# Performance work log

Measured on AMD Instinct MI355X. Metric: run time of the kernel, lower is better.

Reference implementation:

```python
import jax, jax.numpy as jnp
import numpy as np

N = 100000   # total atoms in the batch
E = 400000   # directed edges (bonds both directions)
F = 11       # raw atom feature dim (Linear(11, vector_dim))
D = 512      # vector_dim
L = 5        # num_conv_layers
G = 2048     # number of molecules (graphs) in the batch


def setup_inputs() -> dict:
    key = jax.random.key(0)
    k = jax.random.split(key, 6)
    x = jax.random.uniform(k[0], (N, F), dtype=jnp.float32)  # nonneg counts-like features
    edge_index = jax.random.randint(k[1], (2, E), 0, N, dtype=jnp.int32)
    batch = jnp.sort(jax.random.randint(k[2], (N,), 0, G, dtype=jnp.int32))
    exp_W = jax.random.normal(k[3], (F, D), dtype=jnp.float32) * (1.0 / np.sqrt(F))
    exp_b = jnp.zeros((D,), dtype=jnp.float32)
    gcn_W = jax.random.normal(k[4], (L, D, D), dtype=jnp.float32) * (1.0 / np.sqrt(D))
    gcn_b = jnp.zeros((L, D), dtype=jnp.float32)
    return {"x": x, "edge_index": edge_index, "batch": batch,
            "exp_W": exp_W, "exp_b": exp_b, "gcn_W": gcn_W, "gcn_b": gcn_b}


def reference(x, edge_index, batch, exp_W, exp_b, gcn_W, gcn_b):
    # GraphEmbedding.forward (eval mode: dropout = identity)
    src, dst = edge_index[0], edge_index[1]
    h = jnp.log(x + 1.0) @ exp_W + exp_b  # expansion Linear(11, D)  -> [N, D]

    # GCN normalization with improved=True: self-loop weight 2.0
    # deg_i = sum of incoming edge weights (1.0) + 2.0 self-loop
    ones_e = jnp.ones((E,), dtype=h.dtype)
    deg = jax.ops.segment_sum(ones_e, dst, num_segments=N) + 2.0
    dinv = jax.lax.rsqrt(deg)              # deg >= 2, always finite
    enorm = dinv[src] * dinv[dst]          # per-edge norm (weight 1.0)
    self_norm = 2.0 * dinv * dinv          # self-loop norm (weight 2.0)

    for l in range(L):
        xw = h @ gcn_W[l]                                   # [N, D]
        msg = enorm[:, None] * xw[src]                      # gather + scale, [E, D]
        agg = jax.ops.segment_sum(msg, dst, num_segments=N)  # scatter-add
        agg = agg + self_norm[:, None] * xw + gcn_b[l]
        h = h + jax.nn.relu(agg)                            # residual + relu (dropout off)

    # global_add_pool over molecules
    return jax.ops.segment_sum(h, batch, num_segments=G)    # [G, D]
```

## Files before the change

kernel.cpp:

```cpp
#include <hip/hip_runtime.h>
#include <hip/hip_bf16.h>
#include <stdint.h>

typedef __attribute__((ext_vector_type(8))) short bf16x8;
typedef __attribute__((ext_vector_type(4))) float f32x4;
typedef unsigned short ushort_t;
typedef unsigned int uint_t;

__device__ __forceinline__ unsigned short f2bf(float f) {
  unsigned u = __float_as_uint(f);
  u += 0x7fffu + ((u >> 16) & 1u);
  return (unsigned short)(u >> 16);
}
__device__ __forceinline__ float bf2f(unsigned u16) {
  return __uint_as_float(u16 << 16);
}
__device__ __forceinline__ void fma8(float* a, uint4 u, float w) {
  a[0] += w * bf2f(u.x & 0xffffu); a[1] += w * bf2f(u.x >> 16);
  a[2] += w * bf2f(u.y & 0xffffu); a[3] += w * bf2f(u.y >> 16);
  a[4] += w * bf2f(u.z & 0xffffu); a[5] += w * bf2f(u.z >> 16);
  a[6] += w * bf2f(u.w & 0xffffu); a[7] += w * bf2f(u.w >> 16);
}
__device__ __forceinline__ uint4 pack8u(const float* a) {
  uint4 p;
  p.x = (uint_t)f2bf(a[0]) | ((uint_t)f2bf(a[1]) << 16);
  p.y = (uint_t)f2bf(a[2]) | ((uint_t)f2bf(a[3]) << 16);
  p.z = (uint_t)f2bf(a[4]) | ((uint_t)f2bf(a[5]) << 16);
  p.w = (uint_t)f2bf(a[6]) | ((uint_t)f2bf(a[7]) << 16);
  return p;
}

__global__ void k_zero(int* __restrict__ p, int n) {
  int i = blockIdx.x * blockDim.x + threadIdx.x;
  if (i < n) p[i] = 0;
}

__global__ void k_prep_w(const float* __restrict__ W, ushort_t* __restrict__ Wt, int total) {
  int idx = blockIdx.x * blockDim.x + threadIdx.x;
  if (idx >= total) return;
  int j   = idx & 7;
  int col = (idx >> 3) & 127;
  int kg  = (idx >> 10) & 3;
  int kt  = (idx >> 12) & 15;
  int nt  = (idx >> 16) & 3;
  int l   = idx >> 18;
  int k = kt * 32 + kg * 8 + j;
  int n = nt * 128 + col;
  Wt[idx] = f2bf(W[((size_t)(l * 512 + k)) * 512 + n]);
}

__global__ __launch_bounds__(256) void k_expand(const float* __restrict__ x,
                                                const float* __restrict__ eW,
                                                const float* __restrict__ eb,
                                                ushort_t* __restrict__ h, int N) {
  const int wid = (blockIdx.x * 256 + threadIdx.x) >> 6;
  const int nw = (gridDim.x * 256) >> 6;
  const int l = threadIdx.x & 63;

  float wf[11][8];
  float bias[8];
#pragma unroll
  for (int f = 0; f < 11; ++f) {
    float4 a = *(const float4*)&eW[f * 512 + l * 8];
    float4 b = *(const float4*)&eW[f * 512 + l * 8 + 4];
    wf[f][0] = a.x; wf[f][1] = a.y; wf[f][2] = a.z; wf[f][3] = a.w;
    wf[f][4] = b.x; wf[f][5] = b.y; wf[f][6] = b.z; wf[f][7] = b.w;
  }
  {
    float4 a = *(const float4*)&eb[l * 8];
    float4 b = *(const float4*)&eb[l * 8 + 4];
    bias[0] = a.x; bias[1] = a.y; bias[2] = a.z; bias[3] = a.w;
    bias[4] = b.x; bias[5] = b.y; bias[6] = b.z; bias[7] = b.w;
  }

  for (int n = wid; n < N; n += nw) {
    float xv = (l < 11) ? x[(size_t)n * 11 + l] : 0.f;
    float lx = log1pf(xv);
    float acc[8];
#pragma unroll
    for (int j = 0; j < 8; ++j) acc[j] = bias[j];
#pragma unroll
    for (int f = 0; f < 11; ++f) {
      float c = __shfl(lx, f, 64);
#pragma unroll
      for (int j = 0; j < 8; ++j) acc[j] += c * wf[f][j];
    }
    *(uint4*)(h + (size_t)n * 512 + l * 8) = pack8u(acc);
  }
}

__global__ void k_deg(const int* __restrict__ dst, int* __restrict__ deg, int E) {
  int e = blockIdx.x * blockDim.x + threadIdx.x;
  if (e < E) atomicAdd(&deg[dst[e]], 1);
}

__global__ void k_dinv(const int* __restrict__ deg, float* __restrict__ dinv,
                       float* __restrict__ selfn, int N) {
  int n = blockIdx.x * blockDim.x + threadIdx.x;
  if (n >= N) return;
  float d = (float)deg[n] + 2.0f;
  dinv[n] = rsqrtf(d);
  selfn[n] = 2.0f / d;
}

__global__ void k_scan_a(const int* __restrict__ deg, int* __restrict__ off,
                         int* __restrict__ bsum, int N) {
  __shared__ int sd[256];
  int t = threadIdx.x;
  int i0 = blockIdx.x * 1024 + t * 4;
  int d[4];
#pragma unroll
  for (int j = 0; j < 4; ++j) d[j] = (i0 + j < N) ? deg[i0 + j] : 0;
  int ts = d[0] + d[1] + d[2] + d[3];
  sd[t] = ts;
  __syncthreads();
  for (int o = 1; o < 256; o <<= 1) {
    int v = (t >= o) ? sd[t - o] : 0;
    __syncthreads();
    sd[t] += v;
    __syncthreads();
  }
  int incl = sd[t];
  int run = incl - ts;
#pragma unroll
  for (int j = 0; j < 4; ++j) {
    if (i0 + j < N) off[i0 + j] = run;
    run += d[j];
  }
  if (t == 255) bsum[blockIdx.x] = incl;
}

__global__ void k_scan_b(const int* __restrict__ bsum, int* __restrict__ bpre, int nb,
                         int* __restrict__ off, int N, int E) {
  __shared__ int sd[256];
  int t = threadIdx.x;
  int v = (t < nb) ? bsum[t] : 0;
  sd[t] = v;
  __syncthreads();
  for (int o = 1; o < 256; o <<= 1) {
    int u = (t >= o) ? sd[t - o] : 0;
    __syncthreads();
    sd[t] += u;
    __syncthreads();
  }
  if (t < nb) bpre[t] = sd[t] - v;
  if (t == 0) off[N] = E;
}

__global__ void k_scan_c(int* __restrict__ off, const int* __restrict__ bpre, int N) {
  int i = blockIdx.x * blockDim.x + threadIdx.x;
  if (i < N) off[i] += bpre[i >> 10];
}

__global__ void k_fill(const int* __restrict__ src, const int* __restrict__ dst,
                       const int* __restrict__ off, int* __restrict__ cur,
                       int* __restrict__ ssrc, int E) {
  int e = blockIdx.x * blockDim.x + threadIdx.x;
  if (e >= E) return;
  int t = dst[e];
  int p = atomicAdd(&cur[t], 1);
  ssrc[off[t] + p] = src[e];
}

__global__ __launch_bounds__(256) void k_agg2(const ushort_t* __restrict__ h,
                                              ushort_t* __restrict__ s,
                                              const int* __restrict__ off,
                                              const int* __restrict__ ssrc,
                                              const float* __restrict__ dinv,
                                              const float* __restrict__ selfn, int N) {
  const int wid = (blockIdx.x * 256 + threadIdx.x) >> 6;
  const int nw = (gridDim.x * 256) >> 6;
  const int l = threadIdx.x & 63;

  for (int n0 = wid * 2; n0 < N; n0 += nw * 2) {
    const int n1 = n0 + 1;
    const bool v1 = n1 < N;
    int i0 = off[n0], e0 = off[n0 + 1];
    int i1 = v1 ? e0 : 0, e1 = v1 ? off[n1 + 1] : 0;
    float dn0 = dinv[n0], dn1 = v1 ? dinv[n1] : 0.f;
    float a0[8], a1[8];
    {
      uint4 u = *(const uint4*)(h + (size_t)n0 * 512 + l * 8);
      float sn = selfn[n0];
      a0[0] = sn * bf2f(u.x & 0xffffu); a0[1] = sn * bf2f(u.x >> 16);
      a0[2] = sn * bf2f(u.y & 0xffffu); a0[3] = sn * bf2f(u.y >> 16);
      a0[4] = sn * bf2f(u.z & 0xffffu); a0[5] = sn * bf2f(u.z >> 16);
      a0[6] = sn * bf2f(u.w & 0xffffu); a0[7] = sn * bf2f(u.w >> 16);
    }
#pragma unroll
    for (int j = 0; j < 8; ++j) a1[j] = 0.f;
    if (v1) {
      uint4 u = *(const uint4*)(h + (size_t)n1 * 512 + l * 8);
      fma8(a1, u, selfn[n1]);
    }
    while (i0 < e0 && i1 < e1) {
      int m0 = ssrc[i0++], m1 = ssrc[i1++];
      float w0 = dn0 * dinv[m0], w1 = dn1 * dinv[m1];
      uint4 u0 = *(const uint4*)(h + (size_t)m0 * 512 + l * 8);
      uint4 u1 = *(const uint4*)(h + (size_t)m1 * 512 + l * 8);
      fma8(a0, u0, w0);
      fma8(a1, u1, w1);
    }
    while (i0 < e0) {
      int m0 = ssrc[i0++];
      float w0 = dn0 * dinv[m0];
      uint4 u0 = *(const uint4*)(h + (size_t)m0 * 512 + l * 8);
      fma8(a0, u0, w0);
    }
    while (i1 < e1) {
      int m1 = ssrc[i1++];
      float w1 = dn1 * dinv[m1];
      uint4 u1 = *(const uint4*)(h + (size_t)m1 * 512 + l * 8);
      fma8(a1, u1, w1);
    }
    *(uint4*)(s + (size_t)n0 * 512 + l * 8) = pack8u(a0);
    if (v1) *(uint4*)(s + (size_t)n1 * 512 + l * 8) = pack8u(a1);
  }
}

__global__ __launch_bounds__(256) void k_gemm(const ushort_t* __restrict__ s,
                                              const ushort_t* __restrict__ Wt,
                                              const float* __restrict__ gbl,
                                              ushort_t* __restrict__ h, int N) {
  __shared__ alignas(16) ushort_t smem[8192];
  ushort_t* Alds = smem;
  ushort_t* Blds = smem + 4096;
  const int tid = threadIdx.x;
  const int m0 = blockIdx.x * 128;
  const int nt = blockIdx.y;
  const int wv = tid >> 6, ln = tid & 63;
  const int wrow = wv >> 1, wcol = wv & 1;
  const int l15 = ln & 15, l4 = ln >> 4;

  f32x4 acc[4][4];
#pragma unroll
  for (int i = 0; i < 4; ++i)
#pragma unroll
    for (int j = 0; j < 4; ++j) acc[i][j] = (f32x4){0.f, 0.f, 0.f, 0.f};

  const int arow0 = tid >> 2, apiece = tid & 3;
  const int grow0 = min(m0 + arow0, N - 1);
  const int grow1 = min(m0 + 64 + arow0, N - 1);

  for (int kt = 0; kt < 16; ++kt) {
    __syncthreads();
    {
      const ushort_t* p0 = s + (size_t)grow0 * 512 + kt * 32 + apiece * 8;
      const ushort_t* p1 = s + (size_t)grow1 * 512 + kt * 32 + apiece * 8;
      __builtin_amdgcn_global_load_lds(
          (const __attribute__((address_space(1))) uint_t*)p0,
          (__attribute__((address_space(3))) uint_t*)&Alds[tid * 8], 16, 0, 0);
      __builtin_amdgcn_global_load_lds(
          (const __attribute__((address_space(1))) uint_t*)p1,
          (__attribute__((address_space(3))) uint_t*)&Alds[(256 + tid) * 8], 16, 0, 0);
    }
    {
      const ushort_t* wt = Wt + (((size_t)nt * 16 + kt) << 12);
      const ushort_t* g1 = wt + (tid << 3);
      __builtin_amdgcn_global_load_lds(
          (const __attribute__((address_space(1))) uint_t*)g1,
          (__attribute__((address_space(3))) uint_t*)&Blds[tid * 8], 16, 0, 0);
      __builtin_amdgcn_global_load_lds(
          (const __attribute__((address_space(1))) uint_t*)(g1 + 2048),
          (__attribute__((address_space(3))) uint_t*)&Blds[(256 + tid) * 8], 16, 0, 0);
    }
    __syncthreads();
    bf16x8 a[4], b[4];
#pragma unroll
    for (int i = 0; i < 4; ++i)
      a[i] = *(const bf16x8*)&Alds[(wrow * 64 + i * 16 + l15) * 32 + l4 * 8];
#pragma unroll
    for (int j = 0; j < 4; ++j)
      b[j] = *(const bf16x8*)&Blds[(l4 * 128 + wcol * 64 + j * 16 + l15) * 8];
#pragma unroll
    for (int i = 0; i < 4; ++i)
#pragma unroll
      for (int j = 0; j < 4; ++j)
        acc[i][j] = __builtin_amdgcn_mfma_f32_16x16x32_bf16(a[i], b[j], acc[i][j], 0, 0, 0);
  }

  float* cst = (float*)smem;
  __syncthreads();
#pragma unroll
  for (int p = 0; p < 4; ++p) {
    const int wrow_sel = p >> 1, ipair = (p & 1) * 2;
    if (wrow == wrow_sel) {
#pragma unroll
      for (int ii = 0; ii < 2; ++ii) {
        int i = ipair + ii;
#pragma unroll
        for (int v = 0; v < 4; ++v) {
          int r32 = ii * 16 + l4 * 4 + v;
#pragma unroll
          for (int j = 0; j < 4; ++j)
            cst[r32 * 128 + wcol * 64 + j * 16 + l15] = acc[i][j][v];
        }
      }
    }
    __syncthreads();
#pragma unroll
    for (int k = 0; k < 2; ++k) {
      int u = k * 256 + tid;
      int row_l = u >> 4, cb = u & 15;
      int grow = m0 + wrow_sel * 64 + ipair * 16 + row_l;
      if (grow < N) {
        float4 c0 = *(const float4*)&cst[row_l * 128 + cb * 8];
        float4 c1 = *(const float4*)&cst[row_l * 128 + cb * 8 + 4];
        float c[8] = {c0.x, c0.y, c0.z, c0.w, c1.x, c1.y, c1.z, c1.w};
        const float* gp = gbl + nt * 128 + cb * 8;
        float4 b0 = *(const float4*)gp;
        float4 b1 = *(const float4*)(gp + 4);
        float bb[8] = {b0.x, b0.y, b0.z, b0.w, b1.x, b1.y, b1.z, b1.w};
        ushort_t* hp = h + (size_t)grow * 512 + nt * 128 + cb * 8;
        uint4 hu = *(const uint4*)hp;
        float hv[8];
        hv[0] = bf2f(hu.x & 0xffffu); hv[1] = bf2f(hu.x >> 16);
        hv[2] = bf2f(hu.y & 0xffffu); hv[3] = bf2f(hu.y >> 16);
        hv[4] = bf2f(hu.z & 0xffffu); hv[5] = bf2f(hu.z >> 16);
        hv[6] = bf2f(hu.w & 0xffffu); hv[7] = bf2f(hu.w >> 16);
#pragma unroll
        for (int j = 0; j < 8; ++j) hv[j] += fmaxf(c[j] + bb[j], 0.f);
        *(uint4*)hp = pack8u(hv);
      }
    }
    __syncthreads();
  }
}

__device__ __forceinline__ int lbound(const int* a, int n, int v) {
  int lo = 0, hi = n;
  while (lo < hi) {
    int m = (lo + hi) >> 1;
    if (a[m] < v) lo = m + 1; else hi = m;
  }
  return lo;
}

__global__ __launch_bounds__(256) void k_pool(const ushort_t* __restrict__ h,
                                              const int* __restrict__ batch,
                                              float* __restrict__ out, int N) {
  __shared__ float red[4 * 512];
  int g = blockIdx.x;
  int t = threadIdx.x;
  int w = t >> 6, l = t & 63;
  int start = lbound(batch, N, g);
  int end = lbound(batch, N, g + 1);
  float acc[8];
#pragma unroll
  for (int j = 0; j < 8; ++j) acc[j] = 0.f;
  for (int n = start + w; n < end; n += 4) {
    uint4 u = *(const uint4*)(h + (size_t)n * 512 + l * 8);
    acc[0] += bf2f(u.x & 0xffffu); acc[1] += bf2f(u.x >> 16);
    acc[2] += bf2f(u.y & 0xffffu); acc[3] += bf2f(u.y >> 16);
    acc[4] += bf2f(u.z & 0xffffu); acc[5] += bf2f(u.z >> 16);
    acc[6] += bf2f(u.w & 0xffffu); acc[7] += bf2f(u.w >> 16);
  }
#pragma unroll
  for (int j = 0; j < 8; ++j) red[w * 512 + l * 8 + j] = acc[j];
  __syncthreads();
  if (t < 128) {
    float4 sv = make_float4(0.f, 0.f, 0.f, 0.f);
#pragma unroll
    for (int ww = 0; ww < 4; ++ww) {
      float4 v = *(const float4*)&red[ww * 512 + t * 4];
      sv.x += v.x; sv.y += v.y; sv.z += v.z; sv.w += v.w;
    }
    *(float4*)&out[(size_t)g * 512 + t * 4] = sv;
  }
}

extern "C" void kernel_launch(void* const* d_in, const int* in_sizes, int n_in,
                              void* d_out, int out_size, void* d_ws, size_t ws_size,
                              hipStream_t stream) {
  const float* x  = (const float*)d_in[0];
  const int* ei   = (const int*)d_in[1];
  const int* batch= (const int*)d_in[2];
  const float* eW = (const float*)d_in[3];
  const float* eb = (const float*)d_in[4];
  const float* gW = (const float*)d_in[5];
  const float* gb = (const float*)d_in[6];
  float* out = (float*)d_out;

  const int N = in_sizes[0] / 11;
  const int E = in_sizes[1] / 2;
  const int G = out_size / 512;
  const int L = in_sizes[5] / (512 * 512);

  const int* src = ei;
  const int* dst = ei + E;

  char* p = (char*)d_ws;
  auto carve = [&](size_t bytes) {
    char* q = p;
    p += (bytes + 255) & ~(size_t)255;
    return q;
  };
  ushort_t* h         = (ushort_t*)carve((size_t)N * 512 * 2);
  ushort_t* s         = (ushort_t*)carve((size_t)N * 512 * 2);
  ushort_t* Wt        = (ushort_t*)carve((size_t)L * 512 * 512 * 2);
  int* deg            = (int*)carve((size_t)N * 4);
  float* dinv         = (float*)carve((size_t)N * 4);
  float* selfn        = (float*)carve((size_t)N * 4);
  int* off            = (int*)carve(((size_t)N + 1) * 4);
  int* cur            = (int*)carve((size_t)N * 4);
  int* ssrc           = (int*)carve((size_t)E * 4);
  int* bsum           = (int*)carve(1024);
  int* bpre           = (int*)carve(1024);

  k_zero<<<(N + 255) / 256, 256, 0, stream>>>(deg, N);
  k_zero<<<(N + 255) / 256, 256, 0, stream>>>(cur, N);

  int totW = L * 512 * 512;
  k_prep_w<<<(totW + 255) / 256, 256, 0, stream>>>(gW, Wt, totW);
  k_expand<<<2048, 256, 0, stream>>>(x, eW, eb, h, N);
  k_deg<<<(E + 255) / 256, 256, 0, stream>>>(dst, deg, E);
  k_dinv<<<(N + 255) / 256, 256, 0, stream>>>(deg, dinv, selfn, N);
  int nb = (N + 1023) / 1024;
  k_scan_a<<<nb, 256, 0, stream>>>(deg, off, bsum, N);
  k_scan_b<<<1, 256, 0, stream>>>(bsum, bpre, nb, off, N, E);
  k_scan_c<<<(N + 255) / 256, 256, 0, stream>>>(off, bpre, N);
  k_fill<<<(E + 255) / 256, 256, 0, stream>>>(src, dst, off, cur, ssrc, E);

  dim3 ggrid((N + 127) / 128, 4);
  for (int l = 0; l < L; ++l) {
    k_agg2<<<2048, 256, 0, stream>>>(h, s, off, ssrc, dinv, selfn, N);
    k_gemm<<<ggrid, 256, 0, stream>>>(s, Wt + (size_t)l * 512 * 512,
                                      gb + (size_t)l * 512, h, N);
  }
  k_pool<<<G, 256, 0, stream>>>(h, batch, out, N);
}
```

Measured before the change: 1.237 ms.

## Double-buffer GEMM LDS tiles and swap grid axes for A-tile reuse

The GEMM kernel now uses two LDS buffers so the global-to-LDS loads for the next K tile are issued before the MFMAs on the current tile, with one barrier per iteration instead of two. The A tile layout in LDS changes to a k-group-major arrangement to match the B layout. The grid axes are swapped so the four N-tiles sharing one row block run next to each other, which should improve L2 reuse of the activation rows. LDS use doubles, which may lower occupancy, and the epilogue reuses buffer 0 right after the last barrier.

```diff
diff --git a/kernel.cpp b/kernel.cpp
--- a/kernel.cpp
+++ b/kernel.cpp
@@ -222,12 +222,10 @@
                                               const ushort_t* __restrict__ Wt,
                                               const float* __restrict__ gbl,
                                               ushort_t* __restrict__ h, int N) {
-  __shared__ alignas(16) ushort_t smem[8192];
-  ushort_t* Alds = smem;
-  ushort_t* Blds = smem + 4096;
+  __shared__ alignas(16) ushort_t AB[2][8192];
   const int tid = threadIdx.x;
-  const int m0 = blockIdx.x * 128;
-  const int nt = blockIdx.y;
+  const int nt = blockIdx.x;
+  const int m0 = blockIdx.y * 128;
   const int wv = tid >> 6, ln = tid & 63;
   const int wrow = wv >> 1, wcol = wv & 1;
   const int l15 = ln & 15, l4 = ln >> 4;
@@ -238,49 +236,50 @@
 #pragma unroll
     for (int j = 0; j < 4; ++j) acc[i][j] = (f32x4){0.f, 0.f, 0.f, 0.f};
 
-  const int arow0 = tid >> 2, apiece = tid & 3;
-  const int grow0 = min(m0 + arow0, N - 1);
-  const int grow1 = min(m0 + 64 + arow0, N - 1);
+  const int arow = tid & 127, akg = tid >> 7;
+  const ushort_t* pa = s + (size_t)min(m0 + arow, N - 1) * 512 + akg * 8;
+  const ushort_t* wtb = Wt + ((size_t)nt << 16);
+
+  auto stage = [&](int kt, int buf) {
+    ushort_t* base = &AB[buf][0];
+    const ushort_t* a0 = pa + kt * 32;
+    __builtin_amdgcn_global_load_lds(
+        (const __attribute__((address_space(1))) uint_t*)a0,
+        (__attribute__((address_space(3))) uint_t*)&base[tid * 8], 16, 0, 0);
+    __builtin_amdgcn_global_load_lds(
+        (const __attribute__((address_space(1))) uint_t*)(a0 + 16),
+        (__attribute__((address_space(3))) uint_t*)&base[(256 + tid) * 8], 16, 0, 0);
+    const ushort_t* wt = wtb + (kt << 12);
+    __builtin_amdgcn_global_load_lds(
+        (const __attribute__((address_space(1))) uint_t*)(wt + tid * 8),
+        (__attribute__((address_space(3))) uint_t*)&base[4096 + tid * 8], 16, 0, 0);
+    __builtin_amdgcn_global_load_lds(
+        (const __attribute__((address_space(1))) uint_t*)(wt + (256 + tid) * 8),
+        (__attribute__((address_space(3))) uint_t*)&base[4096 + (256 + tid) * 8], 16, 0, 0);
+  };
+
+  stage(0, 0);
+  __syncthreads();
 
   for (int kt = 0; kt < 16; ++kt) {
-    __syncthreads();
-    {
-      const ushort_t* p0 = s + (size_t)grow0 * 512 + kt * 32 + apiece * 8;
-      const ushort_t* p1 = s + (size_t)grow1 * 512 + kt * 32 + apiece * 8;
-      __builtin_amdgcn_global_load_lds(
-          (const __attribute__((address_space(1))) uint_t*)p0,
-          (__attribute__((address_space(3))) uint_t*)&Alds[tid * 8], 16, 0, 0);
-      __builtin_amdgcn_global_load_lds(
-          (const __attribute__((address_space(1))) uint_t*)p1,
-          (__attribute__((address_space(3))) uint_t*)&Alds[(256 + tid) * 8], 16, 0, 0);
-    }
-    {
-      const ushort_t* wt = Wt + (((size_t)nt * 16 + kt) << 12);
-      const ushort_t* g1 = wt + (tid << 3);
-      __builtin_amdgcn_global_load_lds(
-          (const __attribute__((address_space(1))) uint_t*)g1,
-          (__attribute__((address_space(3))) uint_t*)&Blds[tid * 8], 16, 0, 0);
-      __builtin_amdgcn_global_load_lds(
-          (const __attribute__((address_space(1))) uint_t*)(g1 + 2048),
-          (__attribute__((address_space(3))) uint_t*)&Blds[(256 + tid) * 8], 16, 0, 0);
-    }
-    __syncthreads();
+    const int cur = kt & 1;
+    if (kt < 15) stage(kt + 1, cur ^ 1);
     bf16x8 a[4], b[4];
 #pragma unroll
     for (int i = 0; i < 4; ++i)
-      a[i] = *(const bf16x8*)&Alds[(wrow * 64 + i * 16 + l15) * 32 + l4 * 8];
+      a[i] = *(const bf16x8*)&AB[cur][(l4 * 128 + wrow * 64 + i * 16 + l15) * 8];
 #pragma unroll
     for (int j = 0; j < 4; ++j)
-      b[j] = *(const bf16x8*)&Blds[(l4 * 128 + wcol * 64 + j * 16 + l15) * 8];
+      b[j] = *(const bf16x8*)&AB[cur][4096 + (l4 * 128 + wcol * 64 + j * 16 + l15) * 8];
 #pragma unroll
     for (int i = 0; i < 4; ++i)
 #pragma unroll
       for (int j = 0; j < 4; ++j)
         acc[i][j] = __builtin_amdgcn_mfma_f32_16x16x32_bf16(a[i], b[j], acc[i][j], 0, 0, 0);
-  }
-
-  float* cst = (float*)smem;
-  __syncthreads();
+    __syncthreads();
+  }
+
+  float* cst = (float*)&AB[0][0];
 #pragma unroll
   for (int p = 0; p < 4; ++p) {
     const int wrow_sel = p >> 1, ipair = (p & 1) * 2;
@@ -421,7 +420,7 @@
   k_scan_c<<<(N + 255) / 256, 256, 0, stream>>>(off, bpre, N);
   k_fill<<<(E + 255) / 256, 256, 0, stream>>>(src, dst, off, cur, ssrc, E);
 
-  dim3 ggrid((N + 127) / 128, 4);
+  dim3 ggrid(4, (N + 127) / 128);
   for (int l = 0; l < L; ++l) {
     k_agg2<<<2048, 256, 0, stream>>>(h, s, off, ssrc, dinv, selfn, N);
     k_gemm<<<ggrid, 256, 0, stream>>>(s, Wt + (size_t)l * 512 * 512,
```

After: 1.221 ms. About the same (-1.3%).
